# Kernel optimization log

Measured on AMD Instinct MI355X. Metric: run time of the kernel, lower is better.

Reference implementation:

```python
import jax, jax.numpy as jnp
import numpy as np

N_FRAMES = 4
HEADS = 8
SEQ = 576
DIM = 640


def setup_inputs() -> dict:
    key = jax.random.key(0)
    ks = jax.random.split(key, 6)
    x = jax.random.normal(ks[0], (3 * N_FRAMES, SEQ, DIM), dtype=jnp.float32)
    s = 1.0 / np.sqrt(DIM)
    Wq = jax.random.normal(ks[1], (DIM, DIM), dtype=jnp.float32) * s
    Wk = jax.random.normal(ks[2], (DIM, DIM), dtype=jnp.float32) * s
    Wv = jax.random.normal(ks[3], (DIM, DIM), dtype=jnp.float32) * s
    Wo = jax.random.normal(ks[4], (DIM, DIM), dtype=jnp.float32) * s
    bo = jnp.zeros((DIM,), dtype=jnp.float32)
    return {"x": x, "Wq": Wq, "Wk": Wk, "Wv": Wv, "Wo": Wo, "bo": bo}


def reference(x, Wq, Wk, Wv, Wo, bo):
    # x: [3F, S, D] -- stacked [source | uncond | cond] frame batches
    B, S, D = x.shape
    n = B // 3                       # n_frames
    h = HEADS
    hd = D // h
    scale = 1.0 / jnp.sqrt(jnp.asarray(hd, x.dtype))

    # torch nn.Linear: y = x @ W.T
    q = jnp.einsum('bsd,ed->bse', x, Wq)
    k = jnp.einsum('bsd,ed->bse', x, Wk)
    v = jnp.einsum('bsd,ed->bse', x, Wv)

    def heads_fd(t):  # [F,S,D] -> [F,h,S,hd]
        return t.reshape(t.shape[0], S, h, hd).transpose(0, 2, 1, 3)

    def heads_flat(t):  # [F,S,D] -> [h, F*S, hd]  (shared across all query frames)
        return t.reshape(t.shape[0] * S, h, hd).transpose(1, 0, 2)

    # ---- source: per-frame self-attention ----
    qs, ks_, vs = heads_fd(q[:n]), heads_fd(k[:n]), heads_fd(v[:n])
    sim_s = jnp.einsum('fhqd,fhkd->fhqk', qs, ks_) * scale
    out_s = jnp.einsum('fhqk,fhkd->fhqd', jax.nn.softmax(sim_s, axis=-1), vs)

    # ---- uncond / cond: each frame attends to concatenated KV of all frames ----
    def cross_frame(q_chunk, k_chunk, v_chunk):
        qf = heads_fd(q_chunk)          # [F,h,S,hd]
        kf = heads_flat(k_chunk)        # [h,F*S,hd]
        vf = heads_flat(v_chunk)        # [h,F*S,hd]
        sim = jnp.einsum('fhqd,hkd->fhqk', qf, kf) * scale   # [F,h,S,F*S]
        return jnp.einsum('fhqk,hkd->fhqd', jax.nn.softmax(sim, axis=-1), vf)

    out_u = cross_frame(q[n:2 * n], k[n:2 * n], v[n:2 * n])
    out_c = cross_frame(q[2 * n:], k[2 * n:], v[2 * n:])

    out = jnp.concatenate([out_s, out_u, out_c], axis=0)      # [3F,h,S,hd]
    out = out.transpose(0, 2, 1, 3).reshape(B, S, D)          # merge heads
    return jnp.einsum('bsd,ed->bse', out, Wo) + bo
```

## Files before the change

### kernel.cpp

```cpp
#include <hip/hip_runtime.h>
#include <hip/hip_bf16.h>

#define SEQ    576
#define DIM    640
#define HEADS  8
#define HD     80
#define NF     4
#define NB     12
#define M_TOT  (NB * SEQ)
#define SCALE  0.11180339887498949f
#define LOG2E  1.4426950408889634f

typedef __attribute__((ext_vector_type(8))) short          bf16x8;
typedef __attribute__((ext_vector_type(4))) float          f32x4;
typedef __attribute__((ext_vector_type(8))) unsigned short u16x8;
typedef __attribute__((ext_vector_type(4))) unsigned short u16x4;

__device__ __forceinline__ unsigned short f2bf(float x) {
    unsigned u = __float_as_uint(x);
    u += 0x7fffu + ((u >> 16) & 1u);
    return (unsigned short)(u >> 16);
}
__device__ __forceinline__ float bf2f(unsigned short h) {
    return __uint_as_float((unsigned)h << 16);
}
__device__ __forceinline__ f32x4 mfma16(bf16x8 a, bf16x8 b, f32x4 c) {
    return __builtin_amdgcn_mfma_f32_16x16x32_bf16(a, b, c, 0, 0, 0);
}
__device__ __forceinline__ float fexp2(float x) {
    return __builtin_amdgcn_exp2f(x);
}
__device__ __forceinline__ float max3f(float a, float b, float c) {
    return fmaxf(fmaxf(a, b), c);
}
__device__ __forceinline__ void dma16(const void* g, void* s) {
    __builtin_amdgcn_global_load_lds(
        (const __attribute__((address_space(1))) void*)g,
        (__attribute__((address_space(3))) void*)s, 16, 0, 0);
}

__global__ __launch_bounds__(256) void split_kernel(
    const float* __restrict__ X,  const float* __restrict__ Wq,
    const float* __restrict__ Wk, const float* __restrict__ Wv,
    const float* __restrict__ Wo,
    unsigned short* __restrict__ Xh,  unsigned short* __restrict__ Wqh,
    unsigned short* __restrict__ Wkh, unsigned short* __restrict__ Wvh,
    unsigned short* __restrict__ Woh)
{
    const int z = blockIdx.y;
    const float* src; unsigned short* dh; int n; float s = 1.0f;
    switch (z) {
        case 0:  src = X;  dh = Xh;  n = M_TOT * DIM; break;
        case 1:  src = Wq; dh = Wqh; n = DIM * DIM; s = SCALE * LOG2E; break;
        case 2:  src = Wk; dh = Wkh; n = DIM * DIM; break;
        case 3:  src = Wv; dh = Wvh; n = DIM * DIM; break;
        default: src = Wo; dh = Woh; n = DIM * DIM; break;
    }
    const int base = blockIdx.x * 4096 + threadIdx.x * 16;
    if (base >= n) return;
#pragma unroll
    for (int half = 0; half < 2; ++half) {
        const int b = base + half * 8;
        float4 a4 = *(const float4*)(src + b);
        float4 b4 = *(const float4*)(src + b + 4);
        float vv[8] = {a4.x, a4.y, a4.z, a4.w, b4.x, b4.y, b4.z, b4.w};
        union { unsigned short u[8]; u16x8 v; } ph;
#pragma unroll
        for (int j = 0; j < 8; ++j) ph.u[j] = f2bf(vv[j] * s);
        *(u16x8*)(dh + b) = ph.v;
    }
}

__global__ __launch_bounds__(256) void qkv_mfma_kernel(
    const unsigned short* __restrict__ Xh,
    const unsigned short* __restrict__ Wqh, const unsigned short* __restrict__ Wkh,
    const unsigned short* __restrict__ Wvh,
    unsigned short* __restrict__ Qh,
    unsigned short* __restrict__ Kb, unsigned short* __restrict__ VtG)
{
    __shared__ unsigned short smem[2][6144];

    const int flat = blockIdx.x + 54 * (blockIdx.y + 10 * blockIdx.z);
    const int xcd  = flat & 7;
    const int slot = flat >> 3;
    const int l    = (xcd < 4 ? xcd * 203 : 812 + (xcd - 4) * 202) + slot;
    const int m_idx = l / 30;
    const int rem   = l - m_idx * 30;
    const int z     = rem / 10;
    const int n_idx = rem - z * 10;

    const unsigned short* WH = (z == 0) ? Wqh : ((z == 1) ? Wkh : Wvh);
    const int m0 = m_idx * 128;
    const int n0 = n_idx * 64;

    const int t    = threadIdx.x;
    const int w    = t >> 6;
    const int lane = t & 63;
    const int quad = lane >> 4;
    const int ln   = lane & 15;

    f32x4 acc[2][4];
#pragma unroll
    for (int mi = 0; mi < 2; ++mi)
#pragma unroll
        for (int nt = 0; nt < 4; ++nt)
#pragma unroll
            for (int e = 0; e < 4; ++e) acc[mi][nt][e] = 0.f;

    const int lr = lane >> 2;
    const int lc = (lane & 3) * 8;

    auto stage = [&](int buf, int k0) {
        unsigned short* As = smem[buf];
        unsigned short* Bs = smem[buf] + 4096;
        const unsigned short* gp = Xh + (size_t)(m0 + w * 32 + lr) * DIM + k0 + lc;
#pragma unroll
        for (int i = 0; i < 2; ++i)
            dma16(gp + (size_t)i * 16 * DIM, &As[(w * 32 + i * 16) * 32]);
        const size_t gb = (size_t)(n0 + w * 16 + lr) * DIM + k0 + lc;
        dma16(WH + gb, &Bs[w * 16 * 32]);
    };

    stage(0, 0);
    __syncthreads();

    for (int k0 = 0; k0 < DIM; k0 += 32) {
        const int kb = (k0 >> 5) & 1;
        if (k0 + 32 < DIM) stage(kb ^ 1, k0 + 32);

        const unsigned short* As = smem[kb];
        const unsigned short* Bs = smem[kb] + 4096;
        bf16x8 af[2];
#pragma unroll
        for (int mi = 0; mi < 2; ++mi)
            af[mi] = *(const bf16x8*)&As[(w * 32 + mi * 16 + ln) * 32 + quad * 8];
#pragma unroll
        for (int nt = 0; nt < 4; ++nt) {
            bf16x8 bh = *(const bf16x8*)&Bs[(nt * 16 + ln) * 32 + quad * 8];
#pragma unroll
            for (int mi = 0; mi < 2; ++mi)
                acc[mi][nt] = mfma16(af[mi], bh, acc[mi][nt]);
        }
        __syncthreads();
    }

    if (z == 0) {
#pragma unroll
        for (int mi = 0; mi < 2; ++mi)
#pragma unroll
            for (int r = 0; r < 4; ++r) {
                const size_t row = m0 + w * 32 + mi * 16 + quad * 4 + r;
#pragma unroll
                for (int nt = 0; nt < 4; ++nt)
                    Qh[row * DIM + n0 + nt * 16 + ln] = f2bf(acc[mi][nt][r]);
            }
    } else if (z == 1) {
#pragma unroll
        for (int mi = 0; mi < 2; ++mi)
#pragma unroll
            for (int r = 0; r < 4; ++r) {
                const size_t row = m0 + w * 32 + mi * 16 + quad * 4 + r;
#pragma unroll
                for (int nt = 0; nt < 4; ++nt)
                    Kb[row * DIM + n0 + nt * 16 + ln] = f2bf(acc[mi][nt][r]);
            }
    } else {
        unsigned short* Vts = smem[0];
#pragma unroll
        for (int mi = 0; mi < 2; ++mi)
#pragma unroll
            for (int nt = 0; nt < 4; ++nt)
#pragma unroll
                for (int r = 0; r < 4; ++r)
                    Vts[(nt * 16 + ln) * 136 + w * 32 + mi * 16 + quad * 4 + r] =
                        f2bf(acc[mi][nt][r]);
        __syncthreads();
        const int nn = t & 63;
        const int c0 = (t >> 6) * 32;
#pragma unroll
        for (int i = 0; i < 4; ++i)
            *(u16x8*)(VtG + (size_t)(n0 + nn) * M_TOT + m0 + c0 + i * 8) =
                *(const u16x8*)&Vts[nn * 136 + c0 + i * 8];
    }
}

__global__ __launch_bounds__(256, 2) void attn_mfma_kernel(
    const unsigned short* __restrict__ Qh,
    const unsigned short* __restrict__ Kb, const unsigned short* __restrict__ Vt,
    unsigned short* __restrict__ Oh,
    unsigned short* __restrict__ Pn, float2* __restrict__ ml)
{
    const int flat = blockIdx.x + 3 * (blockIdx.y + 8 * blockIdx.z);
    const int h    = flat & 7;
    const int slot = flat >> 3;
    const int z    = slot / 3;
    const int qt   = slot - z * 3;

    int f, kbase, nkt, idx = -1;
    if (z < 16) {
        idx = z;
        const int fi = z >> 1;
        f = 4 + fi;
        kbase = ((fi < 4 ? 4 : 8) + (z & 1) * 2) * SEQ;
        nkt = 18;
    } else {
        f = z - 16;
        kbase = f * SEQ;
        nkt = 9;
    }

    const int t    = threadIdx.x;
    const int w    = t >> 6;
    const int lane = t & 63;
    const int quad = lane >> 4;
    const int ln   = lane & 15;

    __shared__ unsigned short KhS[2][12 * 64 * 8];
    __shared__ unsigned short VtS[2][96 * 64];

    const int klane = (lane & 3) | (((lane >> 4) & 1) << 2) |
                      (((lane >> 2) & 3) << 3) | (lane & 32);

    auto stage_k = [&](int buf, int kvt) {
        const unsigned short* kg = Kb + (size_t)(kbase + kvt * 64) * DIM + h * HD;
#pragma unroll
        for (int rnd = 0; rnd < 3; ++rnd) {
            const int g = rnd * 4 + w;
            dma16(kg + (size_t)klane * DIM + g * 8, &KhS[buf][g * 512]);
        }
    };
    u16x8 vreg[3];
    auto load_v = [&](int kvt) {
#pragma unroll
        for (int i = 0; i < 3; ++i) {
            const int u = t + i * 256;
            if (u < 640) {
                const int d = u >> 3, c8 = u & 7;
                vreg[i] = *(const u16x8*)(Vt + (size_t)(h * HD + d) * M_TOT +
                                          kbase + kvt * 64 + c8 * 8);
            }
        }
    };
    auto write_v = [&](int buf) {
#pragma unroll
        for (int i = 0; i < 3; ++i) {
            const int u = t + i * 256;
            if (u < 640) {
                const int d = u >> 3, c8 = u & 7;
                const int c8s = (c8 + 3 * d) & 7;
                *(u16x8*)&VtS[buf][d * 64 + c8s * 8] = vreg[i];
            }
        }
    };

    stage_k(0, 0);
    load_v(0);

    {
        const int buf = t >> 7;
        const int c   = t & 127;
        const int row = 80 + (c >> 3);
        const unsigned short val = (row == 80) ? (unsigned short)0x3F80 : (unsigned short)0;
        union { unsigned short u[8]; u16x8 v; } fill;
#pragma unroll
        for (int j = 0; j < 8; ++j) fill.u[j] = val;
        *(u16x8*)&VtS[buf][row * 64 + (c & 7) * 8] = fill.v;
    }

    bf16x8 qf[3][3];
#pragma unroll
    for (int mi = 0; mi < 3; ++mi) {
        const int qrow = f * SEQ + qt * 192 + w * 48 + mi * 16 + ln;
        const unsigned short* qp = Qh + (size_t)qrow * DIM + h * HD;
#pragma unroll
        for (int kc = 0; kc < 3; ++kc) {
            const int dbase = kc * 32 + quad * 8;
            if (dbase < HD) {
                qf[mi][kc] = *(const bf16x8*)(qp + dbase);
            } else {
                union { unsigned short u[8]; bf16x8 v; } zz;
#pragma unroll
                for (int j = 0; j < 8; ++j) zz.u[j] = 0;
                qf[mi][kc] = zz.v;
            }
        }
    }

    float m_[3];
#pragma unroll
    for (int mi = 0; mi < 3; ++mi) m_[mi] = -INFINITY;

    f32x4 oacc[3][6];
#pragma unroll
    for (int mi = 0; mi < 3; ++mi)
#pragma unroll
        for (int nt = 0; nt < 6; ++nt)
#pragma unroll
            for (int e = 0; e < 4; ++e) oacc[mi][nt][e] = 0.f;

    write_v(0);
    __syncthreads();

    for (int kt = 0; kt < nkt; ++kt) {
        const int cur = kt & 1;
        const bool pf = (kt + 1 < nkt);

        if (pf) {
            load_v(kt + 1);
            stage_k(cur ^ 1, kt + 1);
        }

        const f32x4 fz = {0.f, 0.f, 0.f, 0.f};
        f32x4 sacc[3][4];
#pragma unroll
        for (int nt = 0; nt < 4; ++nt) {
            const int ks = ln + 16 * (nt >> 1) + 32 * (nt & 1);
#pragma unroll
            for (int kc = 0; kc < 3; ++kc) {
                bf16x8 kf = *(const bf16x8*)&KhS[cur][((kc * 4 + quad) * 64 + ks) * 8];
#pragma unroll
                for (int mi = 0; mi < 3; ++mi)
                    sacc[mi][nt] = (kc == 0)
                        ? mfma16(kf, qf[mi][0], fz)
                        : mfma16(kf, qf[mi][kc], sacc[mi][nt]);
            }
        }

        float mxl[3];
#pragma unroll
        for (int mi = 0; mi < 3; ++mi) {
            const f32x4* S = sacc[mi];
            const float a = max3f(S[0][0], S[0][1], S[0][2]);
            const float b = max3f(S[0][3], S[1][0], S[1][1]);
            const float c = max3f(S[1][2], S[1][3], S[2][0]);
            const float d = max3f(S[2][1], S[2][2], S[2][3]);
            const float e = max3f(S[3][0], S[3][1], S[3][2]);
            mxl[mi] = fmaxf(max3f(a, b, c), max3f(d, e, S[3][3]));
        }
        const bool need = (mxl[0] > m_[0] + 8.0f) || (mxl[1] > m_[1] + 8.0f) ||
                          (mxl[2] > m_[2] + 8.0f);
        if (__any(need)) {
#pragma unroll
            for (int mi = 0; mi < 3; ++mi) {
                float mx = fmaxf(mxl[mi], __shfl_xor(mxl[mi], 16));
                mx = fmaxf(mx, __shfl_xor(mx, 32));
                const float mnew = fmaxf(m_[mi], mx);
                const float aq = fexp2(m_[mi] - mnew);
                m_[mi] = mnew;
#pragma unroll
                for (int nt = 0; nt < 6; ++nt)
#pragma unroll
                    for (int e = 0; e < 4; ++e) oacc[mi][nt][e] *= aq;
            }
        }
        bf16x8 pfv[3][2];
#pragma unroll
        for (int mi = 0; mi < 3; ++mi) {
            float p[4][4];
#pragma unroll
            for (int nt = 0; nt < 4; ++nt) {
#pragma unroll
                for (int r = 0; r < 4; ++r)
                    p[nt][r] = fexp2(sacc[mi][nt][r] - m_[mi]);
            }
            union { unsigned w[4]; bf16x8 v; } u0, u1;
            u0.w[0] = __builtin_amdgcn_perm(__float_as_uint(p[0][1]),
                                            __float_as_uint(p[0][0]), 0x07060302u);
            u0.w[1] = __builtin_amdgcn_perm(__float_as_uint(p[0][3]),
                                            __float_as_uint(p[0][2]), 0x07060302u);
            u0.w[2] = __builtin_amdgcn_perm(__float_as_uint(p[2][1]),
                                            __float_as_uint(p[2][0]), 0x07060302u);
            u0.w[3] = __builtin_amdgcn_perm(__float_as_uint(p[2][3]),
                                            __float_as_uint(p[2][2]), 0x07060302u);
            u1.w[0] = __builtin_amdgcn_perm(__float_as_uint(p[1][1]),
                                            __float_as_uint(p[1][0]), 0x07060302u);
            u1.w[1] = __builtin_amdgcn_perm(__float_as_uint(p[1][3]),
                                            __float_as_uint(p[1][2]), 0x07060302u);
            u1.w[2] = __builtin_amdgcn_perm(__float_as_uint(p[3][1]),
                                            __float_as_uint(p[3][0]), 0x07060302u);
            u1.w[3] = __builtin_amdgcn_perm(__float_as_uint(p[3][3]),
                                            __float_as_uint(p[3][2]), 0x07060302u);
            pfv[mi][0] = u0.v;
            pfv[mi][1] = u1.v;
        }

#pragma unroll
        for (int kc = 0; kc < 2; ++kc)
#pragma unroll
            for (int nt = 0; nt < 6; ++nt) {
                const int vrow = nt * 16 + ln;
                const int c8r  = ((kc * 4 + quad) + 3 * vrow) & 7;
                bf16x8 vf = *(const bf16x8*)&VtS[cur][vrow * 64 + c8r * 8];
#pragma unroll
                for (int mi = 0; mi < 3; ++mi)
                    oacc[mi][nt] = mfma16(vf, pfv[mi][kc], oacc[mi][nt]);
            }

        if (pf) write_v(cur ^ 1);
        __syncthreads();
    }

#pragma unroll
    for (int mi = 0; mi < 3; ++mi) {
        const float lsum = __shfl(oacc[mi][5][0], ln, 64);
        const float inv = 1.f / lsum;
        const int rr = qt * 192 + w * 48 + mi * 16 + ln;
#pragma unroll
        for (int nt = 0; nt < 5; ++nt) {
            union { unsigned short u[4]; u16x4 v; } o4;
#pragma unroll
            for (int r = 0; r < 4; ++r) o4.u[r] = f2bf(oacc[mi][nt][r] * inv);
            const int dcol = h * HD + nt * 16 + quad * 4;
            if (idx < 0)
                *(u16x4*)&Oh[((size_t)f * SEQ + rr) * DIM + dcol] = o4.v;
            else
                *(u16x4*)&Pn[((size_t)idx * SEQ + rr) * DIM + dcol] = o4.v;
        }
    }
    if (idx >= 0 && lane < 16) {
#pragma unroll
        for (int mi = 0; mi < 3; ++mi) {
            const int rr = qt * 192 + w * 48 + mi * 16 + lane;
            ml[((size_t)idx * 8 + h) * SEQ + rr] =
                make_float2(m_[mi], oacc[mi][5][0]);
        }
    }
}

__global__ __launch_bounds__(320) void merge_kernel(
    const unsigned short* __restrict__ Pn, const float2* __restrict__ ml,
    unsigned short* __restrict__ Oh)
{
    const int row = blockIdx.x;
    const int fi  = blockIdx.y;
    const int t   = threadIdx.x;
    const int i0  = fi * 2, i1 = i0 + 1;
#pragma unroll
    for (int rep = 0; rep < 2; ++rep) {
        const int col = t + rep * 320;
        const int h = col / 80;
        const float2 a = ml[((size_t)i0 * 8 + h) * SEQ + row];
        const float2 b = ml[((size_t)i1 * 8 + h) * SEQ + row];
        const float M  = fmaxf(a.x, b.x);
        const float w0 = fexp2(a.x - M) * a.y;
        const float w1 = fexp2(b.x - M) * b.y;
        const float inv = 1.f / (w0 + w1);
        const float p0 = bf2f(Pn[((size_t)i0 * SEQ + row) * DIM + col]);
        const float p1 = bf2f(Pn[((size_t)i1 * SEQ + row) * DIM + col]);
        Oh[((size_t)(4 + fi) * SEQ + row) * DIM + col] = f2bf((w0 * p0 + w1 * p1) * inv);
    }
}

__global__ __launch_bounds__(256) void oproj_mfma_kernel(
    const unsigned short* __restrict__ Oh,
    const unsigned short* __restrict__ Woh,
    const float* __restrict__ bo, float* __restrict__ out)
{
    __shared__ unsigned short smem[2][6144];

    const int flat = blockIdx.x + 54 * blockIdx.y;
    const int xcd  = flat & 7;
    const int slot = flat >> 3;
    const int l    = (xcd < 4 ? xcd * 68 : 272 + (xcd - 4) * 67) + slot;
    const int m_idx = l / 10;
    const int n_idx = l - m_idx * 10;
    const int m0 = m_idx * 128;
    const int n0 = n_idx * 64;

    const int t    = threadIdx.x;
    const int w    = t >> 6;
    const int lane = t & 63;
    const int quad = lane >> 4;
    const int ln   = lane & 15;

    f32x4 acc[2][4];
#pragma unroll
    for (int mi = 0; mi < 2; ++mi)
#pragma unroll
        for (int nt = 0; nt < 4; ++nt)
#pragma unroll
            for (int e = 0; e < 4; ++e) acc[mi][nt][e] = 0.f;

    const int lr = lane >> 2;
    const int lc = (lane & 3) * 8;

    auto stage = [&](int buf, int k0) {
        unsigned short* As = smem[buf];
        unsigned short* Bs = smem[buf] + 4096;
        const unsigned short* gp = Oh + (size_t)(m0 + w * 32 + lr) * DIM + k0 + lc;
#pragma unroll
        for (int i = 0; i < 2; ++i)
            dma16(gp + (size_t)i * 16 * DIM, &As[(w * 32 + i * 16) * 32]);
        const size_t gb = (size_t)(n0 + w * 16 + lr) * DIM + k0 + lc;
        dma16(Woh + gb, &Bs[w * 16 * 32]);
    };

    stage(0, 0);
    __syncthreads();

    for (int k0 = 0; k0 < DIM; k0 += 32) {
        const int kb = (k0 >> 5) & 1;
        if (k0 + 32 < DIM) stage(kb ^ 1, k0 + 32);

        const unsigned short* As = smem[kb];
        const unsigned short* Bs = smem[kb] + 4096;
        bf16x8 af[2];
#pragma unroll
        for (int mi = 0; mi < 2; ++mi)
            af[mi] = *(const bf16x8*)&As[(w * 32 + mi * 16 + ln) * 32 + quad * 8];
#pragma unroll
        for (int nt = 0; nt < 4; ++nt) {
            bf16x8 bh = *(const bf16x8*)&Bs[(nt * 16 + ln) * 32 + quad * 8];
#pragma unroll
            for (int mi = 0; mi < 2; ++mi)
                acc[mi][nt] = mfma16(af[mi], bh, acc[mi][nt]);
        }
        __syncthreads();
    }

#pragma unroll
    for (int mi = 0; mi < 2; ++mi)
#pragma unroll
        for (int r = 0; r < 4; ++r) {
            const size_t row = m0 + w * 32 + mi * 16 + quad * 4 + r;
#pragma unroll
            for (int nt = 0; nt < 4; ++nt) {
                const int col = n0 + nt * 16 + ln;
                out[row * DIM + col] = acc[mi][nt][r] + bo[col];
            }
        }
}

extern "C" void kernel_launch(void* const* d_in, const int* in_sizes, int n_in,
                              void* d_out, int out_size, void* d_ws, size_t ws_size,
                              hipStream_t stream)
{
    const float* x  = (const float*)d_in[0];
    const float* Wq = (const float*)d_in[1];
    const float* Wk = (const float*)d_in[2];
    const float* Wv = (const float*)d_in[3];
    const float* Wo = (const float*)d_in[4];
    const float* bo = (const float*)d_in[5];
    float* out = (float*)d_out;

    const size_t NX = (size_t)M_TOT * DIM;
    const size_t NW = (size_t)DIM * DIM;
    unsigned short* p = (unsigned short*)d_ws;
    unsigned short* Wqh = p;  p += NW;
    unsigned short* Wkh = p;  p += NW;
    unsigned short* Wvh = p;  p += NW;
    unsigned short* Woh = p;  p += NW;
    unsigned short* Xh  = p;  p += NX;
    unsigned short* Qhb = p;  p += NX;
    unsigned short* Kbb = p;  p += NX;
    unsigned short* Vtb = p;  p += NX;
    unsigned short* Ohb = Xh;

    unsigned short* Pn = (unsigned short*)d_out;
    float2* ml = (float2*)((char*)d_out + (size_t)16 * SEQ * DIM * 2);

    dim3 g0((unsigned)((NX + 4095) / 4096), 5);
    split_kernel<<<g0, 256, 0, stream>>>(x, Wq, Wk, Wv, Wo,
        Xh, Wqh, Wkh, Wvh, Woh);

    dim3 g1(M_TOT / 128, DIM / 64, 3);
    qkv_mfma_kernel<<<g1, 256, 0, stream>>>(Xh, Wqh, Wkh, Wvh, Qhb, Kbb, Vtb);

    dim3 g2(3, HEADS, 20);
    attn_mfma_kernel<<<g2, 256, 0, stream>>>(Qhb, Kbb, Vtb, Ohb, Pn, ml);

    dim3 g3(SEQ, 8);
    merge_kernel<<<g3, 320, 0, stream>>>(Pn, ml, Ohb);

    dim3 g4(M_TOT / 128, DIM / 64);
    oproj_mfma_kernel<<<g4, 256, 0, stream>>>(Ohb, Woh, bo, out);
}
```

Baseline: 185.1 us.

## Fuse split-KV merge into attention kernel via atomic last-block counter

Removes the separate merge kernel: each split-KV attention block bumps an atomic counter per (frame, q-tile, head), and the second finisher merges the two partial outputs using the stored max/sum values. The split kernel is also reshaped into a compact 1D grid so no blocks exit early for the small weight matrices. This saves a kernel launch and a full pass over the partials, but adds a memset, thread fences and a serialized merge tail inside the attention blocks.

Measured after the change: 261.9 us. 1.41x slower.

```diff
diff --git a/kernel.cpp b/kernel.cpp
--- a/kernel.cpp
+++ b/kernel.cpp
@@ -47,27 +47,32 @@
     unsigned short* __restrict__ Wkh, unsigned short* __restrict__ Wvh,
     unsigned short* __restrict__ Woh)
 {
-    const int z = blockIdx.y;
-    const float* src; unsigned short* dh; int n; float s = 1.0f;
-    switch (z) {
-        case 0:  src = X;  dh = Xh;  n = M_TOT * DIM; break;
-        case 1:  src = Wq; dh = Wqh; n = DIM * DIM; s = SCALE * LOG2E; break;
-        case 2:  src = Wk; dh = Wkh; n = DIM * DIM; break;
-        case 3:  src = Wv; dh = Wvh; n = DIM * DIM; break;
-        default: src = Wo; dh = Woh; n = DIM * DIM; break;
-    }
-    const int base = blockIdx.x * 4096 + threadIdx.x * 16;
-    if (base >= n) return;
+    const int b = blockIdx.x;
+    const float* src; unsigned short* dh; int chunk; float s = 1.0f;
+    if (b < 1080) {
+        src = X; dh = Xh; chunk = b;
+    } else {
+        const int wb = b - 1080;
+        const int wsel = wb / 100;
+        chunk = wb - wsel * 100;
+        switch (wsel) {
+            case 0:  src = Wq; dh = Wqh; s = SCALE * LOG2E; break;
+            case 1:  src = Wk; dh = Wkh; break;
+            case 2:  src = Wv; dh = Wvh; break;
+            default: src = Wo; dh = Woh; break;
+        }
+    }
+    const int base = chunk * 4096 + threadIdx.x * 16;
 #pragma unroll
     for (int half = 0; half < 2; ++half) {
-        const int b = base + half * 8;
-        float4 a4 = *(const float4*)(src + b);
-        float4 b4 = *(const float4*)(src + b + 4);
+        const int bb = base + half * 8;
+        float4 a4 = *(const float4*)(src + bb);
+        float4 b4 = *(const float4*)(src + bb + 4);
         float vv[8] = {a4.x, a4.y, a4.z, a4.w, b4.x, b4.y, b4.z, b4.w};
         union { unsigned short u[8]; u16x8 v; } ph;
 #pragma unroll
         for (int j = 0; j < 8; ++j) ph.u[j] = f2bf(vv[j] * s);
-        *(u16x8*)(dh + b) = ph.v;
+        *(u16x8*)(dh + bb) = ph.v;
     }
 }
 
@@ -188,7 +193,8 @@
     const unsigned short* __restrict__ Qh,
     const unsigned short* __restrict__ Kb, const unsigned short* __restrict__ Vt,
     unsigned short* __restrict__ Oh,
-    unsigned short* __restrict__ Pn, float2* __restrict__ ml)
+    unsigned short* __restrict__ Pn, float2* __restrict__ ml,
+    unsigned* __restrict__ cnt)
 {
     const int flat = blockIdx.x + 3 * (blockIdx.y + 8 * blockIdx.z);
     const int h    = flat & 7;
@@ -217,6 +223,7 @@
 
     __shared__ unsigned short KhS[2][12 * 64 * 8];
     __shared__ unsigned short VtS[2][96 * 64];
+    __shared__ int done_s;
 
     const int klane = (lane & 3) | (((lane >> 4) & 1) << 2) |
                       (((lane >> 2) & 3) << 3) | (lane & 32);
@@ -425,29 +432,39 @@
                 make_float2(m_[mi], oacc[mi][5][0]);
         }
     }
-}
-
-__global__ __launch_bounds__(320) void merge_kernel(
-    const unsigned short* __restrict__ Pn, const float2* __restrict__ ml,
-    unsigned short* __restrict__ Oh)
-{
-    const int row = blockIdx.x;
-    const int fi  = blockIdx.y;
-    const int t   = threadIdx.x;
-    const int i0  = fi * 2, i1 = i0 + 1;
-#pragma unroll
-    for (int rep = 0; rep < 2; ++rep) {
-        const int col = t + rep * 320;
-        const int h = col / 80;
-        const float2 a = ml[((size_t)i0 * 8 + h) * SEQ + row];
-        const float2 b = ml[((size_t)i1 * 8 + h) * SEQ + row];
-        const float M  = fmaxf(a.x, b.x);
-        const float w0 = fexp2(a.x - M) * a.y;
-        const float w1 = fexp2(b.x - M) * b.y;
-        const float inv = 1.f / (w0 + w1);
-        const float p0 = bf2f(Pn[((size_t)i0 * SEQ + row) * DIM + col]);
-        const float p1 = bf2f(Pn[((size_t)i1 * SEQ + row) * DIM + col]);
-        Oh[((size_t)(4 + fi) * SEQ + row) * DIM + col] = f2bf((w0 * p0 + w1 * p1) * inv);
+
+    if (idx >= 0) {
+        __threadfence();
+        __syncthreads();
+        if (t == 0)
+            done_s = (int)atomicAdd(&cnt[(z >> 1) * 24 + qt * 8 + h], 1u);
+        __syncthreads();
+        if (done_s == 1) {
+            __threadfence();
+            const int fi = z >> 1;
+            const int i0 = fi * 2, i1 = i0 + 1;
+#pragma unroll
+            for (int i = 0; i < 15; ++i) {
+                const int u   = t + i * 256;
+                const int row = u / 20;
+                const int ch  = u - row * 20;
+                const int rr  = qt * 192 + row;
+                const int col = h * HD + ch * 4;
+                const float2 a = ml[((size_t)i0 * 8 + h) * SEQ + rr];
+                const float2 b = ml[((size_t)i1 * 8 + h) * SEQ + rr];
+                const float M  = fmaxf(a.x, b.x);
+                const float w0 = fexp2(a.x - M) * a.y;
+                const float w1 = fexp2(b.x - M) * b.y;
+                const float inv = 1.f / (w0 + w1);
+                u16x4 q0 = *(const u16x4*)&Pn[((size_t)i0 * SEQ + rr) * DIM + col];
+                u16x4 q1 = *(const u16x4*)&Pn[((size_t)i1 * SEQ + rr) * DIM + col];
+                union { unsigned short us[4]; u16x4 v; } o;
+#pragma unroll
+                for (int j = 0; j < 4; ++j)
+                    o.us[j] = f2bf((w0 * bf2f(q0[j]) + w1 * bf2f(q1[j])) * inv);
+                *(u16x4*)&Oh[((size_t)(4 + fi) * SEQ + rr) * DIM + col] = o.v;
+            }
+        }
     }
 }
 
@@ -555,22 +572,21 @@
     unsigned short* Kbb = p;  p += NX;
     unsigned short* Vtb = p;  p += NX;
     unsigned short* Ohb = Xh;
+    unsigned* cnt = (unsigned*)p;
 
     unsigned short* Pn = (unsigned short*)d_out;
     float2* ml = (float2*)((char*)d_out + (size_t)16 * SEQ * DIM * 2);
 
-    dim3 g0((unsigned)((NX + 4095) / 4096), 5);
-    split_kernel<<<g0, 256, 0, stream>>>(x, Wq, Wk, Wv, Wo,
+    hipMemsetAsync(cnt, 0, 192 * sizeof(unsigned), stream);
+
+    split_kernel<<<dim3(1480), 256, 0, stream>>>(x, Wq, Wk, Wv, Wo,
         Xh, Wqh, Wkh, Wvh, Woh);
 
     dim3 g1(M_TOT / 128, DIM / 64, 3);
     qkv_mfma_kernel<<<g1, 256, 0, stream>>>(Xh, Wqh, Wkh, Wvh, Qhb, Kbb, Vtb);
 
     dim3 g2(3, HEADS, 20);
-    attn_mfma_kernel<<<g2, 256, 0, stream>>>(Qhb, Kbb, Vtb, Ohb, Pn, ml);
-
-    dim3 g3(SEQ, 8);
-    merge_kernel<<<g3, 320, 0, stream>>>(Pn, ml, Ohb);
+    attn_mfma_kernel<<<g2, 256, 0, stream>>>(Qhb, Kbb, Vtb, Ohb, Pn, ml, cnt);
 
     dim3 g4(M_TOT / 128, DIM / 64);
     oproj_mfma_kernel<<<g4, 256, 0, stream>>>(Ohb, Woh, bo, out);
```
